# Kernel optimization log

Hardware: AMD Instinct MI355X
Metric: run time of the kernel (lower is better)

## Reference

```python
import jax, jax.numpy as jnp
import numpy as np

N_NODES = 50000
N_EDGES = 800000
D = 128
L = 2

def mobius_add(x, y, c):
    xy = jnp.sum(x * y, axis=-1, keepdims=True)
    xx = jnp.sum(x * x, axis=-1, keepdims=True)
    yy = jnp.sum(y * y, axis=-1, keepdims=True)
    num = (1 + 2 * c * xy + c * yy) * x + (1 - c * xx) * y
    den = 1 + 2 * c * xy + c * c * xx * yy
    return num / den

def exp_map(x, v, c):
    vn = jnp.linalg.norm(v, axis=-1, keepdims=True)
    sc = jnp.sqrt(c)
    second = jnp.tanh(sc * vn / 2) * v / (sc * vn)
    return mobius_add(x, second, c)

def log_map(x, y, c):
    a = mobius_add(-x, y, c)
    an = jnp.linalg.norm(a, axis=-1, keepdims=True)
    sc = jnp.sqrt(c)
    return 2 / sc * jnp.arctanh(sc * an) * a / an

def l2norm(x, eps=1e-12):
    n = jnp.linalg.norm(x, axis=-1, keepdims=True)
    return x / jnp.maximum(n, eps)

def mean_agg(h, src, dst, n):
    # DGL update_all(copy_u('h','m'), mean('m','neigh')): mean over incoming edges
    s = jax.ops.segment_sum(h[src], dst, num_segments=n)  # [N, D]
    deg = jax.ops.segment_sum(jnp.ones((src.shape[0], 1), h.dtype), dst, num_segments=n)
    return s / jnp.maximum(deg, 1.0)

def setup_inputs() -> dict:
    key = jax.random.key(0)
    ks = jax.random.split(key, 12)
    w_scale = 1.0 / np.sqrt(D)
    return {
        'src': jax.random.randint(ks[0], (N_EDGES,), 0, N_NODES, dtype=jnp.int32),
        'dst': jax.random.randint(ks[1], (N_EDGES,), 0, N_NODES, dtype=jnp.int32),
        'e_emb': jax.random.normal(ks[2], (N_NODES, D), jnp.float32),
        # hyperbolic embeddings must lie well inside the Poincare ball
        'b_emb': jax.random.normal(ks[3], (N_NODES, D), jnp.float32) * 0.004,
        's_emb': jax.random.normal(ks[4], (N_NODES, D), jnp.float32),
        'e_W': jax.random.normal(ks[5], (L, D, D), jnp.float32) * w_scale,
        'e_b': jax.random.normal(ks[6], (L, D), jnp.float32) * 0.01,
        'b_W': jax.random.normal(ks[7], (L, D, D), jnp.float32) * w_scale,
        'b_b': jax.random.normal(ks[8], (L, D), jnp.float32) * 0.01,
        's_W': jax.random.normal(ks[9], (L, D, D), jnp.float32) * w_scale,
        's_b': jax.random.normal(ks[10], (L, D), jnp.float32) * 0.01,
        'b_curv': jnp.ones((1,), jnp.float32),
        's_curv': jnp.ones((1,), jnp.float32),
    }

def reference(src, dst, e_emb, b_emb, s_emb, e_W, e_b, b_W, b_b, s_W, s_b, b_curv, s_curv):
    n = e_emb.shape[0]
    bc = b_curv[0]
    sc = s_curv[0]
    for l in range(L):
        # euclidean: linear -> mean-aggregate -> LeakyReLU(0.2)
        e_h = e_emb @ e_W[l].T + e_b[l]
        e_new = mean_agg(e_h, src, dst, n)
        # hyperbolic: log-map to tangent at origin -> linear -> mean -> exp-map
        origin = jnp.zeros((1, D), b_emb.dtype)
        tang = log_map(origin, b_emb, bc)
        b_h = tang @ b_W[l].T + b_b[l]
        b_agg = mean_agg(b_h, src, dst, n)
        b_new = exp_map(origin, b_agg, bc)
        # spherical: normalize -> linear -> normalize -> mean -> normalize
        s_h = l2norm(s_emb)
        s_h = l2norm(s_h @ s_W[l].T + s_b[l])
        s_new = l2norm(mean_agg(s_h, src, dst, n))
        e_emb = jax.nn.leaky_relu(e_new, 0.2)
        b_emb = b_new
        s_emb = s_new
    return jnp.concatenate([e_emb, b_emb, s_emb], axis=1)  # [N, 3*D]
```

## Files before the change

### kernel.cpp

```cpp
#include <hip/hip_runtime.h>
#include <hip/hip_bf16.h>

#define NN 50000
#define NE 800000
#define DD 128

typedef unsigned int u32;
typedef __attribute__((ext_vector_type(8))) short short8;
typedef __attribute__((ext_vector_type(4))) float f32x4;
typedef __attribute__((ext_vector_type(2))) float f32x2;
typedef __attribute__((ext_vector_type(4))) u32 u32x4;

__device__ __forceinline__ u32 f2bf2(float a, float b){
  union { __hip_bfloat162 h; u32 u; } cv;
  cv.h = __float22bfloat162_rn(make_float2(a, b));
  return cv.u;
}
__device__ __forceinline__ f32x2 up2(u32 v){
  f32x2 r;
  r.x = __uint_as_float(v << 16);
  r.y = __uint_as_float(v & 0xffff0000u);
  return r;
}

struct PrepArgs { const float* W[6]; u32* out; };
__global__ __launch_bounds__(256) void k_prep(PrepArgs pa){
  int tid = blockIdx.x*256 + threadIdx.x;
  int mat = tid >> 11, rem = tid & 2047;
  int frag = rem >> 6, lane = rem & 63;
  int ct = frag >> 2, ks = frag & 3, rr = lane & 15, quad = lane >> 4;
  const float* p = pa.W[mat] + (ct*16 + rr)*128 + ks*32 + quad*8;
  float4 f0 = *(const float4*)p;
  float4 f1 = *(const float4*)(p + 4);
  u32x4 q;
  q.x = f2bf2(f0.x, f0.y); q.y = f2bf2(f0.z, f0.w);
  q.z = f2bf2(f1.x, f1.y); q.w = f2bf2(f1.z, f1.w);
  *(u32x4*)(pa.out + (size_t)tid*4) = q;
}

__global__ void k_hist(const int* __restrict__ dst, int* __restrict__ cnt){
  int i = blockIdx.x*256 + threadIdx.x;
  if (i < NE) atomicAdd(&cnt[dst[i]], 1);
}

__global__ __launch_bounds__(256) void k_alloc(const int* __restrict__ cnt,
                                               int* __restrict__ row_beg,
                                               int* __restrict__ cursor,
                                               int* __restrict__ gcount){
  int i = blockIdx.x*256 + threadIdx.x;
  int lane = threadIdx.x & 63;
  int pc = (i < NN) ? ((cnt[i] + 1) & ~1) : 0;
  int incl = pc;
  #pragma unroll
  for (int off = 1; off < 64; off <<= 1){
    int u = __shfl_up(incl, off, 64);
    if (lane >= off) incl += u;
  }
  int wtot = __shfl(incl, 63, 64);
  int base = 0;
  if (lane == 0) base = atomicAdd(gcount, wtot);
  base = __shfl(base, 0, 64);
  int excl = base + incl - pc;
  if (i < NN){ row_beg[i] = excl; cursor[i] = excl; }
}

__global__ void k_scatter(const int* __restrict__ src, const int* __restrict__ dst,
                          int* __restrict__ cursor, int* __restrict__ esrc){
  int i = blockIdx.x*256 + threadIdx.x;
  if (i < NE){
    int d = dst[i];
    int p = atomicAdd(&cursor[d], 1);
    esrc[p] = (src[i] + 1) * 192;
  }
}

struct GemmArgs {
  const float* A[3];
  const float* Bias[3];
  const u32* Wf;
  u32* H;
  const float* curv;
  int astride;
};

__global__ __launch_bounds__(256,3) void k_gemm(GemmArgs ga){
  const int m = blockIdx.y;
  const float* __restrict__ A    = ga.A[m];
  const float* __restrict__ Bias = ga.Bias[m];
  u32* __restrict__ H = ga.H;
  const int astride = ga.astride;
  const int t = threadIdx.x;
  const int lane = t & 63;
  const int rr = lane & 15, quad = lane >> 4;

  __shared__ u32 Wlds[8192];
  {
    const u32x4* wsrc = (const u32x4*)(ga.Wf + (size_t)m*8192);
    #pragma unroll
    for (int it = 0; it < 8; ++it){
      int idx = it*256 + t;
      *(u32x4*)&Wlds[idx*4] = wsrc[idx];
    }
  }
  __syncthreads();

  float sc = 1.f;
  if (m == 1) sc = sqrtf(*ga.curv);

  const int nw = gridDim.x * 4;
  for (int g = blockIdx.x*4 + (t >> 6); g < 3125; g += nw){
    const float* ap = A + (size_t)(g*16 + rr)*astride + quad*8;
    float4 c[8];
    #pragma unroll
    for (int ks = 0; ks < 4; ++ks){
      c[2*ks]   = *(const float4*)(ap + ks*32);
      c[2*ks+1] = *(const float4*)(ap + ks*32 + 4);
    }
    if (m != 0){
      float p = 0.f;
      #pragma unroll
      for (int i = 0; i < 8; ++i)
        p += c[i].x*c[i].x + c[i].y*c[i].y + c[i].z*c[i].z + c[i].w*c[i].w;
      p += __shfl_xor(p, 16, 64);
      p += __shfl_xor(p, 32, 64);
      float nrm = sqrtf(p);
      float sca;
      if (m == 1){
        float x = sc * nrm;
        sca = (nrm > 1e-30f) ? (logf((1.f + x)/(1.f - x)) / (sc * nrm)) : 2.f;
      } else {
        sca = 1.f / fmaxf(nrm, 1e-12f);
      }
      #pragma unroll
      for (int i = 0; i < 8; ++i){ c[i].x*=sca; c[i].y*=sca; c[i].z*=sca; c[i].w*=sca; }
    }
    f32x4 acc[8];
    #pragma unroll
    for (int ct = 0; ct < 8; ++ct){ f32x4 z = {0.f,0.f,0.f,0.f}; acc[ct] = z; }
    #pragma unroll
    for (int ks = 0; ks < 4; ++ks){
      u32x4 bq;
      bq.x = f2bf2(c[2*ks].x,   c[2*ks].y);
      bq.y = f2bf2(c[2*ks].z,   c[2*ks].w);
      bq.z = f2bf2(c[2*ks+1].x, c[2*ks+1].y);
      bq.w = f2bf2(c[2*ks+1].z, c[2*ks+1].w);
      short8 bf = __builtin_bit_cast(short8, bq);
      #pragma unroll
      for (int ct = 0; ct < 8; ++ct){
        short8 wf = *(const short8*)&Wlds[((ct*4 + ks)*64 + lane)*4];
        acc[ct] = __builtin_amdgcn_mfma_f32_16x16x32_bf16(wf, bf, acc[ct], 0, 0, 0);
      }
    }
    #pragma unroll
    for (int ct = 0; ct < 8; ++ct){
      float4 bv = *(const float4*)(Bias + ct*16 + quad*4);
      acc[ct].x += bv.x; acc[ct].y += bv.y; acc[ct].z += bv.z; acc[ct].w += bv.w;
    }
    if (m == 2){
      float p = 0.f;
      #pragma unroll
      for (int ct = 0; ct < 8; ++ct)
        p += acc[ct].x*acc[ct].x + acc[ct].y*acc[ct].y + acc[ct].z*acc[ct].z + acc[ct].w*acc[ct].w;
      p += __shfl_xor(p, 16, 64);
      p += __shfl_xor(p, 32, 64);
      float inv = 1.f / fmaxf(sqrtf(p), 1e-12f);
      #pragma unroll
      for (int ct = 0; ct < 8; ++ct){ acc[ct].x*=inv; acc[ct].y*=inv; acc[ct].z*=inv; acc[ct].w*=inv; }
    }
    u32* hp = H + (size_t)(g*16 + rr + 1)*192 + m*64 + quad*2;
    #pragma unroll
    for (int ct = 0; ct < 8; ++ct){
      uint2 pk;
      pk.x = f2bf2(acc[ct].x, acc[ct].y);
      pk.y = f2bf2(acc[ct].z, acc[ct].w);
      *(uint2*)(hp + ct*8) = pk;
    }
  }
}

struct FusedArgs {
  const u32* H0;
  u32* H1;
  const int* row_beg;
  const int* cnt;
  const int* esrc;
  const u32* Wf;
  const float* Bias[3];
};

#define NSTR 388

__global__ __launch_bounds__(256,4) void k_fused(FusedArgs fa){
  const int t = threadIdx.x;
  const int w = t >> 6;
  const int lane = t & 63;
  const int half = lane >> 5, hl = lane & 31;
  const int rr = lane & 15, quad = lane >> 4;
  const int nbase = blockIdx.x * 16;

  __shared__ float S[16*NSTR];

  for (int i = 0; i < 4; ++i){
    const int nb = w*4 + i;
    const int node = nbase + nb;
    const int deg = fa.cnt[node];
    const int e0 = fa.row_beg[node];
    const int e1 = e0 + ((deg + 1) & ~1);
    const int* __restrict__ esrc = fa.esrc;
    const u32* __restrict__ Hf = fa.H0 + hl*2;

    f32x2 z2 = {0.f, 0.f};
    f32x2 a0[2] = {z2, z2};
    f32x2 a1[2] = {z2, z2};
    f32x2 a2[2] = {z2, z2};

    for (int base = e0; base < e1; base += 64){
      int nn = e1 - base; if (nn > 64) nn = 64;
      int sv = esrc[min(base + lane, e1 - 1)];
      int np = nn >> 1;
      int p = 0;
      for (; p + 4 <= np; p += 4){
        uint2 q[4][3];
        #pragma unroll
        for (int u = 0; u < 4; ++u){
          int soff = __shfl(sv, 2*(p + u) + half, 64);
          const u32* hp = Hf + soff;
          q[u][0] = *(const uint2*)hp;
          q[u][1] = *(const uint2*)(hp + 64);
          q[u][2] = *(const uint2*)(hp + 128);
        }
        #pragma unroll
        for (int u = 0; u < 4; ++u){
          a0[0] += up2(q[u][0].x); a0[1] += up2(q[u][0].y);
          a1[0] += up2(q[u][1].x); a1[1] += up2(q[u][1].y);
          a2[0] += up2(q[u][2].x); a2[1] += up2(q[u][2].y);
        }
      }
      for (; p < np; ++p){
        int soff = __shfl(sv, 2*p + half, 64);
        const u32* hp = Hf + soff;
        uint2 q0 = *(const uint2*)hp;
        uint2 q1 = *(const uint2*)(hp + 64);
        uint2 q2 = *(const uint2*)(hp + 128);
        a0[0] += up2(q0.x); a0[1] += up2(q0.y);
        a1[0] += up2(q1.x); a1[1] += up2(q1.y);
        a2[0] += up2(q2.x); a2[1] += up2(q2.y);
      }
    }

    #pragma unroll
    for (int j = 0; j < 2; ++j){
      a0[j].x += __shfl_xor(a0[j].x, 32, 64); a0[j].y += __shfl_xor(a0[j].y, 32, 64);
      a1[j].x += __shfl_xor(a1[j].x, 32, 64); a1[j].y += __shfl_xor(a1[j].y, 32, 64);
      a2[j].x += __shfl_xor(a2[j].x, 32, 64); a2[j].y += __shfl_xor(a2[j].y, 32, 64);
    }
    float inv = 1.f / (float)max(deg, 1);
    #pragma unroll
    for (int j = 0; j < 2; ++j){ a0[j] *= inv; a1[j] *= inv; a2[j] *= inv; }

    float p2 = a2[0].x*a2[0].x + a2[0].y*a2[0].y + a2[1].x*a2[1].x + a2[1].y*a2[1].y;
    #pragma unroll
    for (int off = 1; off < 32; off <<= 1) p2 += __shfl_xor(p2, off, 64);
    float s2 = 1.f / fmaxf(sqrtf(p2), 1e-12f);

    float* sp = &S[nb*NSTR];
    if (half == 0){
      f32x4 v0 = { a0[0].x > 0.f ? a0[0].x : 0.2f*a0[0].x,
                   a0[0].y > 0.f ? a0[0].y : 0.2f*a0[0].y,
                   a0[1].x > 0.f ? a0[1].x : 0.2f*a0[1].x,
                   a0[1].y > 0.f ? a0[1].y : 0.2f*a0[1].y };
      *(f32x4*)(sp + hl*4) = v0;
      f32x4 v1 = { a1[0].x, a1[0].y, a1[1].x, a1[1].y };
      *(f32x4*)(sp + 128 + hl*4) = v1;
    } else {
      f32x4 v2 = { a2[0].x*s2, a2[0].y*s2, a2[1].x*s2, a2[1].y*s2 };
      *(f32x4*)(sp + 256 + hl*4) = v2;
    }
  }
  __syncthreads();

  if (w < 3){
    const int m = w;
    short8 bf[4];
    const float* sp = &S[rr*NSTR + m*128];
    #pragma unroll
    for (int ks = 0; ks < 4; ++ks){
      f32x4 lo = *(const f32x4*)(sp + ks*32 + quad*8);
      f32x4 hi = *(const f32x4*)(sp + ks*32 + quad*8 + 4);
      u32x4 bq;
      bq.x = f2bf2(lo.x, lo.y); bq.y = f2bf2(lo.z, lo.w);
      bq.z = f2bf2(hi.x, hi.y); bq.w = f2bf2(hi.z, hi.w);
      bf[ks] = __builtin_bit_cast(short8, bq);
    }
    const u32* __restrict__ wbase = fa.Wf + (size_t)m*8192;
    const float* __restrict__ Bias = fa.Bias[m];
    f32x4 acc[8];
    #pragma unroll
    for (int ct = 0; ct < 8; ++ct){ f32x4 z = {0.f,0.f,0.f,0.f}; acc[ct] = z; }
    #pragma unroll
    for (int ct = 0; ct < 8; ++ct){
      short8 wfr[4];
      #pragma unroll
      for (int ks = 0; ks < 4; ++ks)
        wfr[ks] = *(const short8*)(wbase + ((ct*4 + ks)*64 + lane)*4);
      #pragma unroll
      for (int ks = 0; ks < 4; ++ks)
        acc[ct] = __builtin_amdgcn_mfma_f32_16x16x32_bf16(wfr[ks], bf[ks], acc[ct], 0, 0, 0);
    }
    #pragma unroll
    for (int ct = 0; ct < 8; ++ct){
      float4 bv = *(const float4*)(Bias + ct*16 + quad*4);
      acc[ct].x += bv.x; acc[ct].y += bv.y; acc[ct].z += bv.z; acc[ct].w += bv.w;
    }
    if (m == 2){
      float p = 0.f;
      #pragma unroll
      for (int ct = 0; ct < 8; ++ct)
        p += acc[ct].x*acc[ct].x + acc[ct].y*acc[ct].y + acc[ct].z*acc[ct].z + acc[ct].w*acc[ct].w;
      p += __shfl_xor(p, 16, 64);
      p += __shfl_xor(p, 32, 64);
      float nv = 1.f / fmaxf(sqrtf(p), 1e-12f);
      #pragma unroll
      for (int ct = 0; ct < 8; ++ct){ acc[ct].x*=nv; acc[ct].y*=nv; acc[ct].z*=nv; acc[ct].w*=nv; }
    }
    u32* hp = fa.H1 + (size_t)(nbase + rr + 1)*192 + m*64 + quad*2;
    #pragma unroll
    for (int ct = 0; ct < 8; ++ct){
      uint2 pk;
      pk.x = f2bf2(acc[ct].x, acc[ct].y);
      pk.y = f2bf2(acc[ct].z, acc[ct].w);
      *(uint2*)(hp + ct*8) = pk;
    }
  }
}

struct AggArgs {
  const u32* H;
  float* O;
  const int* row_beg;
  const int* cnt;
  const int* esrc;
  const float* curv;
};

__global__ __launch_bounds__(256) void k_agg(AggArgs aa){
  const int tid = threadIdx.x;
  const int lane = tid & 63;
  const int half = lane >> 5, hl = lane & 31;
  const int node = blockIdx.x*4 + (tid >> 6);
  if (node >= NN) return;
  const int deg = aa.cnt[node];
  const int e0 = aa.row_beg[node];
  const int e1 = e0 + ((deg + 1) & ~1);
  const int* __restrict__ esrc = aa.esrc;
  const u32* __restrict__ Hf = aa.H + hl*2;

  f32x2 z2 = {0.f, 0.f};
  f32x2 a0[2] = {z2, z2};
  f32x2 a1[2] = {z2, z2};
  f32x2 a2[2] = {z2, z2};

  for (int base = e0; base < e1; base += 64){
    int nn = e1 - base; if (nn > 64) nn = 64;
    int sv = esrc[min(base + lane, e1 - 1)];
    int np = nn >> 1;
    int p = 0;
    for (; p + 4 <= np; p += 4){
      uint2 q[4][3];
      #pragma unroll
      for (int u = 0; u < 4; ++u){
        int soff = __shfl(sv, 2*(p + u) + half, 64);
        const u32* hp = Hf + soff;
        q[u][0] = *(const uint2*)hp;
        q[u][1] = *(const uint2*)(hp + 64);
        q[u][2] = *(const uint2*)(hp + 128);
      }
      #pragma unroll
      for (int u = 0; u < 4; ++u){
        a0[0] += up2(q[u][0].x); a0[1] += up2(q[u][0].y);
        a1[0] += up2(q[u][1].x); a1[1] += up2(q[u][1].y);
        a2[0] += up2(q[u][2].x); a2[1] += up2(q[u][2].y);
      }
    }
    for (; p < np; ++p){
      int soff = __shfl(sv, 2*p + half, 64);
      const u32* hp = Hf + soff;
      uint2 q0 = *(const uint2*)hp;
      uint2 q1 = *(const uint2*)(hp + 64);
      uint2 q2 = *(const uint2*)(hp + 128);
      a0[0] += up2(q0.x); a0[1] += up2(q0.y);
      a1[0] += up2(q1.x); a1[1] += up2(q1.y);
      a2[0] += up2(q2.x); a2[1] += up2(q2.y);
    }
  }

  #pragma unroll
  for (int j = 0; j < 2; ++j){
    a0[j].x += __shfl_xor(a0[j].x, 32, 64); a0[j].y += __shfl_xor(a0[j].y, 32, 64);
    a1[j].x += __shfl_xor(a1[j].x, 32, 64); a1[j].y += __shfl_xor(a1[j].y, 32, 64);
    a2[j].x += __shfl_xor(a2[j].x, 32, 64); a2[j].y += __shfl_xor(a2[j].y, 32, 64);
  }
  float inv = 1.f / (float)max(deg, 1);
  #pragma unroll
  for (int j = 0; j < 2; ++j){ a0[j] *= inv; a1[j] *= inv; a2[j] *= inv; }

  float p1 = a1[0].x*a1[0].x + a1[0].y*a1[0].y + a1[1].x*a1[1].x + a1[1].y*a1[1].y;
  float p2 = a2[0].x*a2[0].x + a2[0].y*a2[0].y + a2[1].x*a2[1].x + a2[1].y*a2[1].y;
  #pragma unroll
  for (int off = 1; off < 32; off <<= 1){
    p1 += __shfl_xor(p1, off, 64);
    p2 += __shfl_xor(p2, off, 64);
  }
  float n1 = sqrtf(p1);
  float scv = sqrtf(*aa.curv);
  float x = scv * n1;
  float s1 = (n1 > 1e-30f) ? (tanhf(0.5f*x) / x) : 0.5f;
  float s2 = 1.f / fmaxf(sqrtf(p2), 1e-12f);

  float* op = aa.O + (size_t)node*384;
  if (half == 0){
    float4 e4 = make_float4(a0[0].x > 0.f ? a0[0].x : 0.2f*a0[0].x,
                            a0[0].y > 0.f ? a0[0].y : 0.2f*a0[0].y,
                            a0[1].x > 0.f ? a0[1].x : 0.2f*a0[1].x,
                            a0[1].y > 0.f ? a0[1].y : 0.2f*a0[1].y);
    *(float4*)(op + hl*4) = e4;
    *(float4*)(op + 128 + hl*4) = make_float4(a1[0].x*s1, a1[0].y*s1, a1[1].x*s1, a1[1].y*s1);
  } else {
    *(float4*)(op + 256 + hl*4) = make_float4(a2[0].x*s2, a2[0].y*s2, a2[1].x*s2, a2[1].y*s2);
  }
}

extern "C" void kernel_launch(void* const* d_in, const int* in_sizes, int n_in,
                              void* d_out, int out_size, void* d_ws, size_t ws_size,
                              hipStream_t stream){
  (void)in_sizes; (void)n_in; (void)out_size; (void)ws_size;
  const int*   src    = (const int*)  d_in[0];
  const int*   dst    = (const int*)  d_in[1];
  const float* e_emb  = (const float*)d_in[2];
  const float* b_emb  = (const float*)d_in[3];
  const float* s_emb  = (const float*)d_in[4];
  const float* e_W    = (const float*)d_in[5];
  const float* e_b    = (const float*)d_in[6];
  const float* b_W    = (const float*)d_in[7];
  const float* b_b    = (const float*)d_in[8];
  const float* s_W    = (const float*)d_in[9];
  const float* s_b    = (const float*)d_in[10];
  const float* b_curv = (const float*)d_in[11];
  float* out = (float*)d_out;

  char* ws = (char*)d_ws;
  size_t off = 0;
  auto alloc = [&](size_t bytes) -> void* {
    void* p = (void*)(ws + off);
    off += (bytes + 255) & ~(size_t)255;
    return p;
  };
  int* cnt       = (int*)alloc((size_t)NN*4);
  int* row_beg   = (int*)alloc((size_t)NN*4);
  int* cursor    = (int*)alloc((size_t)NN*4);
  int* gcount    = (int*)alloc(256);
  int* esrc      = (int*)alloc((size_t)(NE + NN + 64)*4);
  u32* h0        = (u32*)alloc((size_t)(NN+1)*192*4);
  u32* h1        = (u32*)alloc((size_t)(NN+1)*192*4);
  u32* wf        = (u32*)alloc((size_t)6*2048*16);

  (void)hipMemsetAsync(cnt, 0, (size_t)NN*4, stream);
  (void)hipMemsetAsync(gcount, 0, 4, stream);
  (void)hipMemsetAsync(esrc, 0, (size_t)(NE + NN + 64)*4, stream);
  (void)hipMemsetAsync(h0, 0, 768, stream);
  (void)hipMemsetAsync(h1, 0, 768, stream);

  PrepArgs pp;
  pp.W[0] = e_W;          pp.W[1] = b_W;          pp.W[2] = s_W;
  pp.W[3] = e_W + 16384;  pp.W[4] = b_W + 16384;  pp.W[5] = s_W + 16384;
  pp.out = wf;
  k_prep   <<<48, 256, 0, stream>>>(pp);

  k_hist   <<<NE/256, 256, 0, stream>>>(dst, cnt);
  k_alloc  <<<(NN+255)/256, 256, 0, stream>>>(cnt, row_beg, cursor, gcount);
  k_scatter<<<NE/256, 256, 0, stream>>>(src, dst, cursor, esrc);

  GemmArgs g;
  g.H = h0; g.curv = b_curv; g.astride = DD;
  g.A[0]=e_emb; g.A[1]=b_emb; g.A[2]=s_emb;
  g.Bias[0]=e_b; g.Bias[1]=b_b; g.Bias[2]=s_b;
  g.Wf = wf;
  k_gemm<<<dim3(157,3), 256, 0, stream>>>(g);

  FusedArgs f;
  f.H0 = h0; f.H1 = h1;
  f.row_beg = row_beg; f.cnt = cnt; f.esrc = esrc;
  f.Wf = wf + 3*8192;
  f.Bias[0] = e_b + DD; f.Bias[1] = b_b + DD; f.Bias[2] = s_b + DD;
  k_fused<<<NN/16, 256, 0, stream>>>(f);

  AggArgs a;
  a.H = h1; a.O = out; a.row_beg = row_beg; a.cnt = cnt; a.esrc = esrc; a.curv = b_curv;
  k_agg<<<(NN + 3)/4, 256, 0, stream>>>(a);
}
```

Measured before the change: 465.8 us.

## Merge prep/hist and gemm/scatter kernels using per-edge atomic rank

Fuses weight prep with the degree histogram into one launch. The histogram atomic now records each edge's rank within its destination, so the CSR scatter no longer needs a second atomic pass over a cursor array; it computes its position as row_beg plus rank. The scatter is folded into the first-layer GEMM launch as extra blocks, cutting two kernel launches and letting the scatter overlap with the GEMM. It adds an extra 3.2MB rank array write and read, and the scatter blocks inherit the GEMM's launch bounds and LDS allocation.

```diff
diff --git a/kernel.cpp b/kernel.cpp
--- a/kernel.cpp
+++ b/kernel.cpp
@@ -23,29 +23,32 @@
   return r;
 }
 
-struct PrepArgs { const float* W[6]; u32* out; };
-__global__ __launch_bounds__(256) void k_prep(PrepArgs pa){
-  int tid = blockIdx.x*256 + threadIdx.x;
-  int mat = tid >> 11, rem = tid & 2047;
-  int frag = rem >> 6, lane = rem & 63;
-  int ct = frag >> 2, ks = frag & 3, rr = lane & 15, quad = lane >> 4;
-  const float* p = pa.W[mat] + (ct*16 + rr)*128 + ks*32 + quad*8;
-  float4 f0 = *(const float4*)p;
-  float4 f1 = *(const float4*)(p + 4);
-  u32x4 q;
-  q.x = f2bf2(f0.x, f0.y); q.y = f2bf2(f0.z, f0.w);
-  q.z = f2bf2(f1.x, f1.y); q.w = f2bf2(f1.z, f1.w);
-  *(u32x4*)(pa.out + (size_t)tid*4) = q;
-}
-
-__global__ void k_hist(const int* __restrict__ dst, int* __restrict__ cnt){
-  int i = blockIdx.x*256 + threadIdx.x;
-  if (i < NE) atomicAdd(&cnt[dst[i]], 1);
+struct InitArgs { const float* W[6]; u32* out; const int* dst; int* cnt; int* rank; };
+__global__ __launch_bounds__(256) void k_init(InitArgs ia){
+  const int bx = blockIdx.x;
+  if (bx < 48){
+    int tid = bx*256 + threadIdx.x;
+    int mat = tid >> 11, rem = tid & 2047;
+    int frag = rem >> 6, lane = rem & 63;
+    int ct = frag >> 2, ks = frag & 3, rr = lane & 15, quad = lane >> 4;
+    const float* p = ia.W[mat] + (ct*16 + rr)*128 + ks*32 + quad*8;
+    float4 f0 = *(const float4*)p;
+    float4 f1 = *(const float4*)(p + 4);
+    u32x4 q;
+    q.x = f2bf2(f0.x, f0.y); q.y = f2bf2(f0.z, f0.w);
+    q.z = f2bf2(f1.x, f1.y); q.w = f2bf2(f1.z, f1.w);
+    *(u32x4*)(ia.out + (size_t)tid*4) = q;
+  } else {
+    int i = (bx - 48)*256 + threadIdx.x;
+    if (i < NE){
+      int d = ia.dst[i];
+      ia.rank[i] = atomicAdd(&ia.cnt[d], 1);
+    }
+  }
 }
 
 __global__ __launch_bounds__(256) void k_alloc(const int* __restrict__ cnt,
                                                int* __restrict__ row_beg,
-                                               int* __restrict__ cursor,
                                                int* __restrict__ gcount){
   int i = blockIdx.x*256 + threadIdx.x;
   int lane = threadIdx.x & 63;
@@ -61,41 +64,46 @@
   if (lane == 0) base = atomicAdd(gcount, wtot);
   base = __shfl(base, 0, 64);
   int excl = base + incl - pc;
-  if (i < NN){ row_beg[i] = excl; cursor[i] = excl; }
-}
-
-__global__ void k_scatter(const int* __restrict__ src, const int* __restrict__ dst,
-                          int* __restrict__ cursor, int* __restrict__ esrc){
-  int i = blockIdx.x*256 + threadIdx.x;
-  if (i < NE){
-    int d = dst[i];
-    int p = atomicAdd(&cursor[d], 1);
-    esrc[p] = (src[i] + 1) * 192;
-  }
-}
-
-struct GemmArgs {
+  if (i < NN) row_beg[i] = excl;
+}
+
+struct MainArgs {
   const float* A[3];
   const float* Bias[3];
   const u32* Wf;
   u32* H;
   const float* curv;
-  int astride;
+  const int* src;
+  const int* dst;
+  const int* rank;
+  const int* row_beg;
+  int* esrc;
 };
 
-__global__ __launch_bounds__(256,3) void k_gemm(GemmArgs ga){
-  const int m = blockIdx.y;
-  const float* __restrict__ A    = ga.A[m];
-  const float* __restrict__ Bias = ga.Bias[m];
-  u32* __restrict__ H = ga.H;
-  const int astride = ga.astride;
+#define GEMM_BLKS 471
+
+__global__ __launch_bounds__(256,3) void k_main(MainArgs ma){
+  const int bx = blockIdx.x;
+  if (bx >= GEMM_BLKS){
+    int i = (bx - GEMM_BLKS)*256 + threadIdx.x;
+    if (i < NE){
+      int d = ma.dst[i];
+      ma.esrc[ma.row_beg[d] + ma.rank[i]] = (ma.src[i] + 1) * 192;
+    }
+    return;
+  }
+  const int m  = bx / 157;
+  const int gx = bx % 157;
+  const float* __restrict__ A    = ma.A[m];
+  const float* __restrict__ Bias = ma.Bias[m];
+  u32* __restrict__ H = ma.H;
   const int t = threadIdx.x;
   const int lane = t & 63;
   const int rr = lane & 15, quad = lane >> 4;
 
   __shared__ u32 Wlds[8192];
   {
-    const u32x4* wsrc = (const u32x4*)(ga.Wf + (size_t)m*8192);
+    const u32x4* wsrc = (const u32x4*)(ma.Wf + (size_t)m*8192);
     #pragma unroll
     for (int it = 0; it < 8; ++it){
       int idx = it*256 + t;
@@ -105,11 +113,11 @@
   __syncthreads();
 
   float sc = 1.f;
-  if (m == 1) sc = sqrtf(*ga.curv);
-
-  const int nw = gridDim.x * 4;
-  for (int g = blockIdx.x*4 + (t >> 6); g < 3125; g += nw){
-    const float* ap = A + (size_t)(g*16 + rr)*astride + quad*8;
+  if (m == 1) sc = sqrtf(*ma.curv);
+
+  const int nw = 157*4;
+  for (int g = gx*4 + (t >> 6); g < 3125; g += nw){
+    const float* ap = A + (size_t)(g*16 + rr)*DD + quad*8;
     float4 c[8];
     #pragma unroll
     for (int ks = 0; ks < 4; ++ks){
@@ -457,7 +465,7 @@
   };
   int* cnt       = (int*)alloc((size_t)NN*4);
   int* row_beg   = (int*)alloc((size_t)NN*4);
-  int* cursor    = (int*)alloc((size_t)NN*4);
+  int* rank      = (int*)alloc((size_t)NE*4);
   int* gcount    = (int*)alloc(256);
   int* esrc      = (int*)alloc((size_t)(NE + NN + 64)*4);
   u32* h0        = (u32*)alloc((size_t)(NN+1)*192*4);
@@ -470,22 +478,20 @@
   (void)hipMemsetAsync(h0, 0, 768, stream);
   (void)hipMemsetAsync(h1, 0, 768, stream);
 
-  PrepArgs pp;
-  pp.W[0] = e_W;          pp.W[1] = b_W;          pp.W[2] = s_W;
-  pp.W[3] = e_W + 16384;  pp.W[4] = b_W + 16384;  pp.W[5] = s_W + 16384;
-  pp.out = wf;
-  k_prep   <<<48, 256, 0, stream>>>(pp);
-
-  k_hist   <<<NE/256, 256, 0, stream>>>(dst, cnt);
-  k_alloc  <<<(NN+255)/256, 256, 0, stream>>>(cnt, row_beg, cursor, gcount);
-  k_scatter<<<NE/256, 256, 0, stream>>>(src, dst, cursor, esrc);
-
-  GemmArgs g;
-  g.H = h0; g.curv = b_curv; g.astride = DD;
-  g.A[0]=e_emb; g.A[1]=b_emb; g.A[2]=s_emb;
-  g.Bias[0]=e_b; g.Bias[1]=b_b; g.Bias[2]=s_b;
-  g.Wf = wf;
-  k_gemm<<<dim3(157,3), 256, 0, stream>>>(g);
+  InitArgs ia;
+  ia.W[0] = e_W;          ia.W[1] = b_W;          ia.W[2] = s_W;
+  ia.W[3] = e_W + 16384;  ia.W[4] = b_W + 16384;  ia.W[5] = s_W + 16384;
+  ia.out = wf; ia.dst = dst; ia.cnt = cnt; ia.rank = rank;
+  k_init<<<48 + (NE+255)/256, 256, 0, stream>>>(ia);
+
+  k_alloc<<<(NN+255)/256, 256, 0, stream>>>(cnt, row_beg, gcount);
+
+  MainArgs m;
+  m.A[0]=e_emb; m.A[1]=b_emb; m.A[2]=s_emb;
+  m.Bias[0]=e_b; m.Bias[1]=b_b; m.Bias[2]=s_b;
+  m.Wf = wf; m.H = h0; m.curv = b_curv;
+  m.src = src; m.dst = dst; m.rank = rank; m.row_beg = row_beg; m.esrc = esrc;
+  k_main<<<GEMM_BLKS + (NE+255)/256, 256, 0, stream>>>(m);
 
   FusedArgs f;
   f.H0 = h0; f.H1 = h1;
```

After: 433.9 us. 6.8% less time.
